# Kernel tuning notes

Hardware: AMD Instinct MI355X
Metric: run time of the kernel (lower is better)

## Reference

```python
import jax, jax.numpy as jnp
import numpy as np

EPS = 1e-12

def _normalize(v):
    n = jnp.linalg.norm(v, axis=-1, keepdims=True)
    return v / jnp.maximum(n, EPS)

def _bgs(J):
    # J: [b, N, D, 3, 2] -> rotation matrices R [b, N, D, 3, 3]
    b1 = _normalize(J[..., :, 0])
    a2 = J[..., :, 1]
    dot = jnp.sum(b1 * a2, axis=-1, keepdims=True)
    b2 = _normalize(a2 - dot * b1)
    b3 = jnp.cross(b1, b2)
    return jnp.stack([b1, b2, b3], axis=-1)  # columns b1,b2,b3

def setup_inputs() -> dict:
    key = jax.random.key(0)
    k1, k2, k3, k4, k5 = jax.random.split(key, 5)
    B, N, D, OUT = 16, 4096, 64, 64
    X = jax.random.normal(k1, (B, N, D, 3), dtype=jnp.float32)
    J = jax.random.normal(k2, (B, N, D, 3, 2), dtype=jnp.float32)
    A = jax.random.normal(k3, (OUT, D), dtype=jnp.float32)
    Bm = jax.random.normal(k4, (OUT, D), dtype=jnp.float32)
    C = jax.random.normal(k5, (OUT, D), dtype=jnp.float32)
    return {"X": X, "J": J, "A": A, "Bm": Bm, "C": C}

def reference(X, J, A, Bm, C):
    R = _bgs(J)  # [b, N, D, 3, 3]
    # RT_i . X == column i of R dotted with X -> scalar per channel
    RTX = jnp.einsum('bndij,bndi->bndj', R, X)  # [b, N, D, 3], j-th entry = RT_j X
    rt0 = RTX[..., 0:1]
    rt1 = RTX[..., 1:2]
    rt2 = RTX[..., 2:3]
    col0 = R[..., :, 0]
    col1 = R[..., :, 1]
    col2 = R[..., :, 2]
    # a_term (after adding b_term, as in original forward)
    a_term = col1 * rt1 + col2 * rt2 + col2 * rt1 - col1 * rt2  # [b, N, D, 3]
    c_term = col0 * rt0
    Y = jnp.einsum('fe,bnei->bnfi', A, a_term) + jnp.einsum('fe,bnei->bnfi', C, c_term)
    Y = jnp.einsum('fe,bnei->bnfi', Bm, Y)
    return Y
```

## Files before the change

kernel.cpp:

```cpp
#include <hip/hip_runtime.h>


typedef __bf16 bf16x8 __attribute__((ext_vector_type(8)));
typedef float floatx4 __attribute__((ext_vector_type(4)));

#define RSW 68

__global__ __launch_bounds__(256) void prep_kernel(const float* __restrict__ A,
                                                   const float* __restrict__ Bm,
                                                   const float* __restrict__ C,
                                                   __bf16* __restrict__ acat) {
    int tid = blockIdx.x * 256 + threadIdx.x;
    int f = tid >> 6;
    int e = tid & 63;
    float m = 0.f, m2 = 0.f;
    #pragma unroll 8
    for (int k = 0; k < 64; ++k) {
        float b = Bm[f * 64 + k];
        m  = fmaf(b, A[k * 64 + e], m);
        m2 = fmaf(b, C[k * 64 + e], m2);
    }
    acat[f * 128 + 2 * e]     = (__bf16)m;
    acat[f * 128 + 2 * e + 1] = (__bf16)m2;
}

static __device__ __forceinline__ unsigned pk(float a, float c) {
    unsigned short ua = __builtin_bit_cast(unsigned short, (__bf16)a);
    unsigned short uc = __builtin_bit_cast(unsigned short, (__bf16)c);
    return ((unsigned)uc << 16) | ua;
}

__global__ __launch_bounds__(256, 3) void main_kernel(const float* __restrict__ X,
                                                      const float* __restrict__ J,
                                                      const __bf16* __restrict__ acat,
                                                      float* __restrict__ out) {
    __shared__ __align__(16) float buf[4][3120];

    const int wave = threadIdx.x >> 6;
    const int lane = threadIdx.x & 63;
    const int l15  = lane & 15;
    const int quad = lane >> 4;
    const int pbase = blockIdx.x * 16 + wave * 4;

    float* stg = buf[wave];

    {
        const floatx4* jg = (const floatx4*)(J + (size_t)pbase * 384);
        const floatx4* xg = (const floatx4*)(X + (size_t)pbase * 192);
        floatx4 jt[6], xt[3];
        #pragma unroll
        for (int t = 0; t < 6; ++t) jt[t] = jg[t * 64 + lane];
        #pragma unroll
        for (int t = 0; t < 3; ++t) xt[t] = xg[t * 64 + lane];
        floatx4* sj = (floatx4*)stg;
        floatx4* sx = (floatx4*)(stg + 1536);
        #pragma unroll
        for (int t = 0; t < 6; ++t) sj[t * 64 + lane] = jt[t];
        #pragma unroll
        for (int t = 0; t < 3; ++t) sx[t * 64 + lane] = xt[t];
    }

    __asm__ volatile("s_waitcnt lgkmcnt(0)" ::: "memory");

    unsigned* zw = (unsigned*)(stg + 2304);

    #pragma unroll
    for (int pi = 0; pi < 4; ++pi) {
        const float* jst = stg + pi * 384 + lane * 6;
        float2 ja = *(const float2*)(jst);
        float2 jb = *(const float2*)(jst + 2);
        float2 jc = *(const float2*)(jst + 4);
        const float* xst = stg + 1536 + pi * 192 + lane * 3;
        float xx = xst[0], xy = xst[1], xz = xst[2];

        float a0x = ja.x, a0y = jb.x, a0z = jc.x;
        float a1x = ja.y, a1y = jb.y, a1z = jc.y;

        float n0 = sqrtf(a0x * a0x + a0y * a0y + a0z * a0z);
        float r0 = 1.0f / fmaxf(n0, 1e-12f);
        float b1x = a0x * r0, b1y = a0y * r0, b1z = a0z * r0;

        float d  = b1x * a1x + b1y * a1y + b1z * a1z;
        float ux = a1x - d * b1x, uy = a1y - d * b1y, uz = a1z - d * b1z;
        float n2 = sqrtf(ux * ux + uy * uy + uz * uz);
        float r2 = 1.0f / fmaxf(n2, 1e-12f);
        float b2x = ux * r2, b2y = uy * r2, b2z = uz * r2;

        float b3x = b1y * b2z - b1z * b2y;
        float b3y = b1z * b2x - b1x * b2z;
        float b3z = b1x * b2y - b1y * b2x;

        float rt0 = b1x * xx + b1y * xy + b1z * xz;
        float rt1 = b2x * xx + b2y * xy + b2z * xz;
        float rt2 = b3x * xx + b3y * xy + b3z * xz;

        float s = rt1 - rt2, t = rt1 + rt2;

        unsigned* zr = zw + (pi * 3) * RSW;
        zr[lane]           = pk(b2x * s + b3x * t, b1x * rt0);
        zr[RSW + lane]     = pk(b2y * s + b3y * t, b1y * rt0);
        zr[2 * RSW + lane] = pk(b2z * s + b3z * t, b1z * rt0);
    }

    bf16x8 afrag[4][4];
    #pragma unroll
    for (int mt = 0; mt < 4; ++mt)
        #pragma unroll
        for (int kc = 0; kc < 4; ++kc)
            afrag[mt][kc] = *(const bf16x8*)(acat + (mt * 16 + l15) * 128 + kc * 32 + quad * 8);

    __asm__ volatile("s_waitcnt lgkmcnt(0)" ::: "memory");

    floatx4 acc[4];
    #pragma unroll
    for (int mt = 0; mt < 4; ++mt) acc[mt] = (floatx4){0.f, 0.f, 0.f, 0.f};

    int row = l15 > 11 ? 11 : l15;
    #pragma unroll
    for (int kc = 0; kc < 4; ++kc) {
        bf16x8 b = *(const bf16x8*)((const __bf16*)zw + row * 136 + kc * 32 + quad * 8);
        #pragma unroll
        for (int mt = 0; mt < 4; ++mt)
            acc[mt] = __builtin_amdgcn_mfma_f32_16x16x32_bf16(afrag[mt][kc], b, acc[mt], 0, 0, 0);
    }

    __asm__ volatile("s_waitcnt lgkmcnt(0)" ::: "memory");

    float* dl = stg;
    #pragma unroll
    for (int mt = 0; mt < 4; ++mt) {
        int n = l15;
        if (n < 12) {
            int pl = (n * 21846) >> 16;
            int i  = n - pl * 3;
            float* dst = dl + pl * 196 + i;
            #pragma unroll
            for (int r = 0; r < 4; ++r) {
                int f = mt * 16 + quad * 4 + r;
                dst[f * 3] = acc[mt][r];
            }
        }
    }

    __asm__ volatile("s_waitcnt lgkmcnt(0)" ::: "memory");

    floatx4* og = (floatx4*)(out + (size_t)pbase * 192);
    #pragma unroll
    for (int t = 0; t < 3; ++t) {
        int g  = t * 64 + lane;
        int pg = (g * 1366) >> 16;
        int o  = g - pg * 48;
        og[g] = *(const floatx4*)(dl + pg * 196 + o * 4);
    }
}

extern "C" void kernel_launch(void* const* d_in, const int* in_sizes, int n_in,
                              void* d_out, int out_size, void* d_ws, size_t ws_size,
                              hipStream_t stream) {
    const float* X  = (const float*)d_in[0];
    const float* J  = (const float*)d_in[1];
    const float* A  = (const float*)d_in[2];
    const float* Bm = (const float*)d_in[3];
    const float* C  = (const float*)d_in[4];
    float* out = (float*)d_out;
    __bf16* acat = (__bf16*)d_ws;

    prep_kernel<<<16, 256, 0, stream>>>(A, Bm, C, acat);

    main_kernel<<<4096, 256, 0, stream>>>(X, J, acat, out);
}
```

Before: 210.4 us.

## Make main kernel persistent over four tiles with register prefetch of next J/X

Each block now handles four 16-point tiles in a loop instead of one, with the grid cut to a quarter. The next tile's J and X are loaded into registers while the current tile is computed, and LDS reads of the next point are software-pipelined. The LDS footprint shrinks by reusing the staging area for the packed Z rows, which allows a higher occupancy target. The aim is to hide global load latency and cut per-block launch overhead. The costs are more register pressure and fewer blocks to spread across CUs.

```diff
diff --git a/kernel.cpp b/kernel.cpp
--- a/kernel.cpp
+++ b/kernel.cpp
@@ -30,127 +30,161 @@
     return ((unsigned)uc << 16) | ua;
 }
 
-__global__ __launch_bounds__(256, 3) void main_kernel(const float* __restrict__ X,
+__global__ __launch_bounds__(256, 4) void main_kernel(const float* __restrict__ X,
                                                       const float* __restrict__ J,
                                                       const __bf16* __restrict__ acat,
                                                       float* __restrict__ out) {
-    __shared__ __align__(16) float buf[4][3120];
+    __shared__ __align__(16) float buf[4][2304];
 
     const int wave = threadIdx.x >> 6;
     const int lane = threadIdx.x & 63;
     const int l15  = lane & 15;
     const int quad = lane >> 4;
-    const int pbase = blockIdx.x * 16 + wave * 4;
+    const int pb0  = blockIdx.x * 64 + wave * 4;
 
     float* stg = buf[wave];
 
+    floatx4 jt[6], xt[3];
     {
-        const floatx4* jg = (const floatx4*)(J + (size_t)pbase * 384);
-        const floatx4* xg = (const floatx4*)(X + (size_t)pbase * 192);
-        floatx4 jt[6], xt[3];
-        #pragma unroll
-        for (int t = 0; t < 6; ++t) jt[t] = jg[t * 64 + lane];
-        #pragma unroll
-        for (int t = 0; t < 3; ++t) xt[t] = xg[t * 64 + lane];
-        floatx4* sj = (floatx4*)stg;
-        floatx4* sx = (floatx4*)(stg + 1536);
-        #pragma unroll
-        for (int t = 0; t < 6; ++t) sj[t * 64 + lane] = jt[t];
-        #pragma unroll
-        for (int t = 0; t < 3; ++t) sx[t * 64 + lane] = xt[t];
+        const floatx4* jg = (const floatx4*)(J + (size_t)pb0 * 384);
+        const floatx4* xg = (const floatx4*)(X + (size_t)pb0 * 192);
+        #pragma unroll
+        for (int u = 0; u < 6; ++u) jt[u] = jg[u * 64 + lane];
+        #pragma unroll
+        for (int u = 0; u < 3; ++u) xt[u] = xg[u * 64 + lane];
     }
 
-    __asm__ volatile("s_waitcnt lgkmcnt(0)" ::: "memory");
-
-    unsigned* zw = (unsigned*)(stg + 2304);
-
     #pragma unroll
-    for (int pi = 0; pi < 4; ++pi) {
-        const float* jst = stg + pi * 384 + lane * 6;
-        float2 ja = *(const float2*)(jst);
-        float2 jb = *(const float2*)(jst + 2);
-        float2 jc = *(const float2*)(jst + 4);
-        const float* xst = stg + 1536 + pi * 192 + lane * 3;
-        float xx = xst[0], xy = xst[1], xz = xst[2];
-
-        float a0x = ja.x, a0y = jb.x, a0z = jc.x;
-        float a1x = ja.y, a1y = jb.y, a1z = jc.y;
-
-        float n0 = sqrtf(a0x * a0x + a0y * a0y + a0z * a0z);
-        float r0 = 1.0f / fmaxf(n0, 1e-12f);
-        float b1x = a0x * r0, b1y = a0y * r0, b1z = a0z * r0;
-
-        float d  = b1x * a1x + b1y * a1y + b1z * a1z;
-        float ux = a1x - d * b1x, uy = a1y - d * b1y, uz = a1z - d * b1z;
-        float n2 = sqrtf(ux * ux + uy * uy + uz * uz);
-        float r2 = 1.0f / fmaxf(n2, 1e-12f);
-        float b2x = ux * r2, b2y = uy * r2, b2z = uz * r2;
-
-        float b3x = b1y * b2z - b1z * b2y;
-        float b3y = b1z * b2x - b1x * b2z;
-        float b3z = b1x * b2y - b1y * b2x;
-
-        float rt0 = b1x * xx + b1y * xy + b1z * xz;
-        float rt1 = b2x * xx + b2y * xy + b2z * xz;
-        float rt2 = b3x * xx + b3y * xy + b3z * xz;
-
-        float s = rt1 - rt2, t = rt1 + rt2;
-
-        unsigned* zr = zw + (pi * 3) * RSW;
-        zr[lane]           = pk(b2x * s + b3x * t, b1x * rt0);
-        zr[RSW + lane]     = pk(b2y * s + b3y * t, b1y * rt0);
-        zr[2 * RSW + lane] = pk(b2z * s + b3z * t, b1z * rt0);
-    }
-
-    bf16x8 afrag[4][4];
-    #pragma unroll
-    for (int mt = 0; mt < 4; ++mt)
-        #pragma unroll
-        for (int kc = 0; kc < 4; ++kc)
-            afrag[mt][kc] = *(const bf16x8*)(acat + (mt * 16 + l15) * 128 + kc * 32 + quad * 8);
-
-    __asm__ volatile("s_waitcnt lgkmcnt(0)" ::: "memory");
-
-    floatx4 acc[4];
-    #pragma unroll
-    for (int mt = 0; mt < 4; ++mt) acc[mt] = (floatx4){0.f, 0.f, 0.f, 0.f};
-
-    int row = l15 > 11 ? 11 : l15;
-    #pragma unroll
-    for (int kc = 0; kc < 4; ++kc) {
-        bf16x8 b = *(const bf16x8*)((const __bf16*)zw + row * 136 + kc * 32 + quad * 8);
+    for (int t = 0; t < 4; ++t) {
+        const int pbase = pb0 + t * 16;
+
+        {
+            floatx4* sj = (floatx4*)stg;
+            floatx4* sx = (floatx4*)(stg + 1536);
+            #pragma unroll
+            for (int u = 0; u < 6; ++u) sj[u * 64 + lane] = jt[u];
+            #pragma unroll
+            for (int u = 0; u < 3; ++u) sx[u * 64 + lane] = xt[u];
+        }
+
+        if (t < 3) {
+            const floatx4* jg = (const floatx4*)(J + (size_t)(pbase + 16) * 384);
+            const floatx4* xg = (const floatx4*)(X + (size_t)(pbase + 16) * 192);
+            #pragma unroll
+            for (int u = 0; u < 6; ++u) jt[u] = jg[u * 64 + lane];
+            #pragma unroll
+            for (int u = 0; u < 3; ++u) xt[u] = xg[u * 64 + lane];
+        }
+
+        __asm__ volatile("s_waitcnt lgkmcnt(0)" ::: "memory");
+
+        float2 ja, jb, jc; float xx, xy, xz;
+        {
+            const float* jst = stg + lane * 6;
+            ja = *(const float2*)(jst);
+            jb = *(const float2*)(jst + 2);
+            jc = *(const float2*)(jst + 4);
+            const float* xst = stg + 1536 + lane * 3;
+            xx = xst[0]; xy = xst[1]; xz = xst[2];
+        }
+        #pragma unroll
+        for (int pi = 0; pi < 4; ++pi) {
+            float2 na = ja, nb = jb, nc = jc; float nx = xx, ny = xy, nz = xz;
+            if (pi < 3) {
+                const float* jst = stg + (pi + 1) * 384 + lane * 6;
+                na = *(const float2*)(jst);
+                nb = *(const float2*)(jst + 2);
+                nc = *(const float2*)(jst + 4);
+                const float* xst = stg + 1536 + (pi + 1) * 192 + lane * 3;
+                nx = xst[0]; ny = xst[1]; nz = xst[2];
+            }
+
+            float a0x = ja.x, a0y = jb.x, a0z = jc.x;
+            float a1x = ja.y, a1y = jb.y, a1z = jc.y;
+
+            float n0 = sqrtf(a0x * a0x + a0y * a0y + a0z * a0z);
+            float r0 = 1.0f / fmaxf(n0, 1e-12f);
+            float b1x = a0x * r0, b1y = a0y * r0, b1z = a0z * r0;
+
+            float d  = b1x * a1x + b1y * a1y + b1z * a1z;
+            float ux = a1x - d * b1x, uy = a1y - d * b1y, uz = a1z - d * b1z;
+            float n2 = sqrtf(ux * ux + uy * uy + uz * uz);
+            float r2 = 1.0f / fmaxf(n2, 1e-12f);
+            float b2x = ux * r2, b2y = uy * r2, b2z = uz * r2;
+
+            float b3x = b1y * b2z - b1z * b2y;
+            float b3y = b1z * b2x - b1x * b2z;
+            float b3z = b1x * b2y - b1y * b2x;
+
+            float rt0 = b1x * xx + b1y * xy + b1z * xz;
+            float rt1 = b2x * xx + b2y * xy + b2z * xz;
+            float rt2 = b3x * xx + b3y * xy + b3z * xz;
+
+            float s = rt1 - rt2, tt = rt1 + rt2;
+
+            unsigned* zr = (unsigned*)(stg + pi * 396);
+            zr[lane]           = pk(b2x * s + b3x * tt, b1x * rt0);
+            zr[RSW + lane]     = pk(b2y * s + b3y * tt, b1y * rt0);
+            zr[2 * RSW + lane] = pk(b2z * s + b3z * tt, b1z * rt0);
+
+            ja = na; jb = nb; jc = nc; xx = nx; xy = ny; xz = nz;
+        }
+
+        __asm__ volatile("s_waitcnt lgkmcnt(0)" ::: "memory");
+
+        const __bf16* ap = acat;
+        __asm__ volatile("" : "+s"(ap));
+        bf16x8 afrag[4][4];
         #pragma unroll
         for (int mt = 0; mt < 4; ++mt)
-            acc[mt] = __builtin_amdgcn_mfma_f32_16x16x32_bf16(afrag[mt][kc], b, acc[mt], 0, 0, 0);
-    }
-
-    __asm__ volatile("s_waitcnt lgkmcnt(0)" ::: "memory");
-
-    float* dl = stg;
-    #pragma unroll
-    for (int mt = 0; mt < 4; ++mt) {
-        int n = l15;
-        if (n < 12) {
-            int pl = (n * 21846) >> 16;
-            int i  = n - pl * 3;
-            float* dst = dl + pl * 196 + i;
-            #pragma unroll
-            for (int r = 0; r < 4; ++r) {
-                int f = mt * 16 + quad * 4 + r;
-                dst[f * 3] = acc[mt][r];
+            #pragma unroll
+            for (int kc = 0; kc < 4; ++kc)
+                afrag[mt][kc] = *(const bf16x8*)(ap + (mt * 16 + l15) * 128 + kc * 32 + quad * 8);
+
+        floatx4 acc[4];
+        #pragma unroll
+        for (int mt = 0; mt < 4; ++mt) acc[mt] = (floatx4){0.f, 0.f, 0.f, 0.f};
+
+        int row = l15 > 11 ? 11 : l15;
+        int pz  = (row * 21846) >> 16;
+        int iz  = row - pz * 3;
+        const __bf16* zb = (const __bf16*)stg + pz * 792 + iz * 136;
+        #pragma unroll
+        for (int kc = 0; kc < 4; ++kc) {
+            bf16x8 b = *(const bf16x8*)(zb + kc * 32 + quad * 8);
+            #pragma unroll
+            for (int mt = 0; mt < 4; ++mt)
+                acc[mt] = __builtin_amdgcn_mfma_f32_16x16x32_bf16(afrag[mt][kc], b, acc[mt], 0, 0, 0);
+        }
+
+        __asm__ volatile("s_waitcnt lgkmcnt(0)" ::: "memory");
+
+        float* dl = stg;
+        #pragma unroll
+        for (int mt = 0; mt < 4; ++mt) {
+            int n = l15;
+            if (n < 12) {
+                int pl = (n * 21846) >> 16;
+                int i  = n - pl * 3;
+                float* dst = dl + pl * 196 + i;
+                #pragma unroll
+                for (int r = 0; r < 4; ++r) {
+                    int f = mt * 16 + quad * 4 + r;
+                    dst[f * 3] = acc[mt][r];
+                }
             }
         }
-    }
-
-    __asm__ volatile("s_waitcnt lgkmcnt(0)" ::: "memory");
-
-    floatx4* og = (floatx4*)(out + (size_t)pbase * 192);
-    #pragma unroll
-    for (int t = 0; t < 3; ++t) {
-        int g  = t * 64 + lane;
-        int pg = (g * 1366) >> 16;
-        int o  = g - pg * 48;
-        og[g] = *(const floatx4*)(dl + pg * 196 + o * 4);
+
+        __asm__ volatile("s_waitcnt lgkmcnt(0)" ::: "memory");
+
+        floatx4* og = (floatx4*)(out + (size_t)pbase * 192);
+        #pragma unroll
+        for (int u = 0; u < 3; ++u) {
+            int g  = u * 64 + lane;
+            int pg = (g * 1366) >> 16;
+            int o  = g - pg * 48;
+            og[g] = *(const floatx4*)(dl + pg * 196 + o * 4);
+        }
     }
 }
 
@@ -167,5 +201,5 @@
 
     prep_kernel<<<16, 256, 0, stream>>>(A, Bm, C, acat);
 
-    main_kernel<<<4096, 256, 0, stream>>>(X, J, acat, out);
-}
+    main_kernel<<<1024, 256, 0, stream>>>(X, J, acat, out);
+}
```

After: 218.8 us. 4.0% more time.
